# Kernel optimization log

Measured on AMD Instinct MI355X. Metric: run time of the kernel, lower is better.

## Reference

```python
import jax, jax.numpy as jnp
import numpy as np

C = 512        # channels
CTX = 768      # context_dim


def setup_inputs() -> dict:
    key = jax.random.key(0)
    ks = jax.random.split(key, 10)
    B, H, W = 8, 64, 64
    Lc = 512
    s = 0.02
    return {
        "x": jax.random.normal(ks[0], (B, C, H, W), jnp.float32),
        "context": jax.random.normal(ks[1], (B, Lc, CTX), jnp.float32),
        "Wq": jax.random.normal(ks[2], (C, C), jnp.float32) * s,
        "bq": jnp.zeros((C,), jnp.float32),
        "Wk": jax.random.normal(ks[3], (CTX, C), jnp.float32) * s,
        "bk": jnp.zeros((C,), jnp.float32),
        "Wv": jax.random.normal(ks[4], (CTX, C), jnp.float32) * s,
        "bv": jnp.zeros((C,), jnp.float32),
        "Wo": jax.random.normal(ks[5], (C, C), jnp.float32) * s,
        "bo": jnp.zeros((C,), jnp.float32),
    }


def reference(x, context, Wq, bq, Wk, bk, Wv, bv, Wo, bo):
    B, Cdim, H, W = x.shape
    scale = Cdim ** (-0.5)
    # [B, HW, C]
    xr = x.reshape(B, Cdim, H * W).transpose(0, 2, 1)
    q = xr @ Wq + bq                      # [B, HW, C]
    k = context @ Wk + bk                 # [B, Lc, C]
    v = context @ Wv + bv                 # [B, Lc, C]
    sim = jnp.einsum('bqc,bkc->bqk', q, k) * scale
    attn = jax.nn.softmax(sim, axis=-1)
    out = jnp.einsum('bqk,bkc->bqc', attn, v)
    out = out @ Wo + bo                   # [B, HW, C]
    out = out.transpose(0, 2, 1).reshape(B, Cdim, H, W)
    return x + out
```

## Files before the change

### kernel.cpp

```cpp
#include <hip/hip_runtime.h>
#include <hip/hip_bf16.h>

typedef __bf16 bf16_t;
typedef bf16_t bf16x8 __attribute__((ext_vector_type(8)));
typedef bf16_t bf16x4 __attribute__((ext_vector_type(4)));
typedef float  f32x4  __attribute__((ext_vector_type(4)));

constexpr int B_ = 8, C_ = 512, HW_ = 4096, LC_ = 512, CTX_ = 768;


__global__ void k_transpose_w3(const float* __restrict__ Wq, const float* __restrict__ Wk,
                               const float* __restrict__ Wo,
                               bf16_t* __restrict__ Wq_t, bf16_t* __restrict__ Wk_t,
                               bf16_t* __restrict__ Wo_t) {
    __shared__ float t[32][33];
    int zz = blockIdx.z;
    const float* in = (zz == 0) ? Wq : (zz == 1) ? Wk : Wo;
    bf16_t* out     = (zz == 0) ? Wq_t : (zz == 1) ? Wk_t : Wo_t;
    int R = (zz == 1) ? CTX_ : C_;
    int r0 = blockIdx.x * 32, c0 = blockIdx.y * 32;
    if (r0 >= R) return;
    int tx = threadIdx.x, ty = threadIdx.y;
#pragma unroll
    for (int i = 0; i < 4; ++i)
        t[ty + i * 8][tx] = in[(size_t)(r0 + ty + i * 8) * C_ + c0 + tx];
    __syncthreads();
#pragma unroll
    for (int i = 0; i < 4; ++i)
        out[(size_t)(c0 + ty + i * 8) * R + r0 + tx] = (bf16_t)t[tx][ty + i * 8];
}

__global__ void k_bias(const float* __restrict__ bk, const float* __restrict__ bv,
                       const bf16_t* __restrict__ Wo_t, const float* __restrict__ bo,
                       float* __restrict__ bkvo) {
    int blk = blockIdx.x, tid = threadIdx.x;
    if (blk >= 128) {
        int i = (blk - 128) * 256 + tid;
        bkvo[i] = bk[i];
        return;
    }
    int wave = tid >> 6, lane = tid & 63;
    int cc = blk * 4 + wave;
    bf16x8 w = *(const bf16x8*)&Wo_t[(size_t)cc * C_ + lane * 8];
    float s = 0.f;
#pragma unroll
    for (int j = 0; j < 8; ++j) s += bv[lane * 8 + j] * (float)w[j];
#pragma unroll
    for (int o = 32; o > 0; o >>= 1) s += __shfl_xor(s, o);
    if (lane == 0) bkvo[512 + cc] = s + bo[cc];
}

__global__ void k_f32_to_bf16(const float* __restrict__ in, bf16_t* __restrict__ out, int n) {
    int i = (blockIdx.x * 256 + threadIdx.x) * 4;
    if (i >= n) return;
    f32x4 v = *(const f32x4*)(in + i);
    bf16x4 w;
    w[0] = (bf16_t)v.x; w[1] = (bf16_t)v.y; w[2] = (bf16_t)v.z; w[3] = (bf16_t)v.w;
    *(bf16x4*)(out + i) = w;
}

template <int MODE>
__global__ __launch_bounds__(256) void k_gemm(
    const bf16_t* __restrict__ A, int lda, long sA,
    const bf16_t* __restrict__ Bt, int ldb, long sB,
    const float* __restrict__ bias,
    void* __restrict__ out_, long sOut,
    int N, int K, float scale) {
    __shared__ bf16_t lA[128 * 32];
    __shared__ bf16_t lB[128 * 32];
    const int z = blockIdx.z;
    A  += (size_t)z * sA;
    Bt += (size_t)z * sB;
    const int tid  = threadIdx.x;
    const int lane = tid & 63;
    const int wave = tid >> 6;
    const int wm = (wave >> 1) * 64, wn = (wave & 1) * 64;
    const int bm0 = blockIdx.y * 128, bn0 = blockIdx.x * 128;
    const int ar = lane & 15, kc = lane >> 4;

    auto lA3 = (__attribute__((address_space(3))) char*)&lA[0];
    auto lB3 = (__attribute__((address_space(3))) char*)&lB[0];

    f32x4 acc[4][4] = {};

    for (int k0 = 0; k0 < K; k0 += 32) {
        __syncthreads();
#pragma unroll
        for (int s = 0; s < 2; ++s) {
            int wchunk = wave * 2 + s;
            int id = wchunk * 64 + lane;
            int row = id >> 2, c4 = id & 3;
            __builtin_amdgcn_global_load_lds(
                (const __attribute__((address_space(1))) void*)
                    &A[(size_t)(bm0 + row) * lda + k0 + c4 * 8],
                (__attribute__((address_space(3))) void*)(lA3 + wchunk * 1024),
                16, 0, 0);
            __builtin_amdgcn_global_load_lds(
                (const __attribute__((address_space(1))) void*)
                    &Bt[(size_t)(bn0 + row) * ldb + k0 + c4 * 8],
                (__attribute__((address_space(3))) void*)(lB3 + wchunk * 1024),
                16, 0, 0);
        }
        __syncthreads();
        bf16x8 af[4], bfr[4];
#pragma unroll
        for (int f = 0; f < 4; ++f) {
            af[f]  = *(const bf16x8*)&lA[(wm + f * 16 + ar) * 32 + kc * 8];
            bfr[f] = *(const bf16x8*)&lB[(wn + f * 16 + ar) * 32 + kc * 8];
        }
#pragma unroll
        for (int fm = 0; fm < 4; ++fm)
#pragma unroll
            for (int fn = 0; fn < 4; ++fn)
                acc[fm][fn] = __builtin_amdgcn_mfma_f32_16x16x32_bf16(
                    af[fm], bfr[fn], acc[fm][fn], 0, 0, 0);
    }

    const int rj = (lane >> 4) * 4;
    const int cj = lane & 15;

#pragma unroll
    for (int fm = 0; fm < 4; ++fm) {
#pragma unroll
        for (int fn = 0; fn < 4; ++fn) {
            int r0 = bm0 + wm + fm * 16 + rj;
            int cc = bn0 + wn + fn * 16 + cj;
            if constexpr (MODE == 3) {
                bf16_t* out = (bf16_t*)out_;
                bf16x4 v;
#pragma unroll
                for (int j = 0; j < 4; ++j) v[j] = (bf16_t)acc[fm][fn][j];
                *(bf16x4*)&out[(size_t)cc * sOut + r0] = v;
            } else {
                float bb = bias[cc];
                if (cc < 512) {
                    bf16_t* o = (bf16_t*)out_;
#pragma unroll
                    for (int j = 0; j < 4; ++j)
                        o[(size_t)(r0 + j) * 512 + cc] = (bf16_t)(acc[fm][fn][j] + bb);
                } else {
                    bf16_t* o = (bf16_t*)out_ + (size_t)B_ * LC_ * C_;
                    int b = r0 >> 9, l0 = r0 & 511;
                    bf16x4 v;
#pragma unroll
                    for (int j = 0; j < 4; ++j) v[j] = (bf16_t)(acc[fm][fn][j] + bb);
                    *(bf16x4*)&o[((size_t)b * C_ + (cc - 512)) * LC_ + l0] = v;
                }
            }
        }
    }
}

#define SWZ(c16, row) ((((c16)) & 56) | (((c16) ^ (row) ^ ((row) >> 3)) & 7))
__global__ __launch_bounds__(512, 2) void k_flash(
    const bf16_t* __restrict__ Wq_t, const float* __restrict__ bq,
    const bf16_t* __restrict__ Kb, const bf16_t* __restrict__ Vt,
    const float* __restrict__ x, float* __restrict__ out) {
    __shared__ bf16_t lQP[64 * 512];
    __shared__ bf16_t lS[3][16384];
    float (*redA)[64] = (float(*)[64])&lQP[0];
    float (*redB)[64] = (float(*)[64])&lQP[1024];

    const int bid = blockIdx.x;
    const int z = bid & 7;
    const int q0 = (bid >> 3) * 64;
    const int tid = threadIdx.x;
    const int lane = tid & 63;
    const int wave = tid >> 6;
    const int wm2 = wave >> 2;
    const int wn4 = wave & 3;
    const int h = lane >> 4;
    const int r15 = lane & 15;

    const bf16_t* Kz = Kb + (size_t)z * LC_ * C_;
    const bf16_t* Vz = Vt + (size_t)z * C_ * LC_;
    const float*  xz = x + (size_t)z * C_ * HW_;

    auto lS3 = (__attribute__((address_space(3))) char*)&lS[0][0];

    auto STAGE = [&](int b, const bf16_t* __restrict__ src, int t) {
#pragma unroll
        for (int s = 0; s < 4; ++s) {
            int id = s * 512 + tid;
            int row = id >> 2, c4 = id & 3;
            int c4s = c4 ^ ((row >> 1) & 3);
            __builtin_amdgcn_global_load_lds(
                (const __attribute__((address_space(1))) void*)
                    &src[(size_t)row * 512 + t * 32 + c4s * 8],
                (__attribute__((address_space(3))) void*)
                    (lS3 + b * 32768 + s * 8192 + wave * 1024),
                16, 0, 0);
        }
    };

    f32x4 acc[2][8];

    auto PHASE = [&](const bf16_t* __restrict__ src, int off) {
        for (int t = 0; t < 16; ++t) {
            if (t <= 13) STAGE((t + 2 + off) % 3, src, t + 2);
            bf16x8 af[2], bfr[8];
            int c16 = t * 4 + h;
#pragma unroll
            for (int m = 0; m < 2; ++m) {
                int row = wm2 * 32 + m * 16 + r15;
                af[m] = *(const bf16x8*)&lQP[row * 512 + SWZ(c16, row) * 8];
            }
            const bf16_t* lb = &lS[(t + off) % 3][0];
#pragma unroll
            for (int n = 0; n < 8; ++n) {
                int row = wn4 * 128 + n * 16 + r15;
                bfr[n] = *(const bf16x8*)&lb[row * 32 + ((h ^ (row >> 1)) & 3) * 8];
            }
            __builtin_amdgcn_s_setprio(1);
#pragma unroll
            for (int m = 0; m < 2; ++m)
#pragma unroll
                for (int n = 0; n < 8; ++n)
                    acc[m][n] = __builtin_amdgcn_mfma_f32_16x16x32_bf16(
                        af[m], bfr[n], acc[m][n], 0, 0, 0);
            __builtin_amdgcn_s_setprio(0);
            if (t < 15) {
                if (t <= 13) asm volatile("s_waitcnt vmcnt(4)" ::: "memory");
                else         asm volatile("s_waitcnt vmcnt(0)" ::: "memory");
                __builtin_amdgcn_sched_barrier(0);
                __builtin_amdgcn_s_barrier();
                __builtin_amdgcn_sched_barrier(0);
            }
        }
    };

    STAGE(0, Wq_t, 0); STAGE(1, Wq_t, 1);
#pragma unroll
    for (int i = 0; i < 16; ++i) {
        int c = i * 32 + (tid >> 4);
        int q = (tid & 15) * 4;
        f32x4 v = *(const f32x4*)&xz[(size_t)c * HW_ + q0 + q];
        int c16 = c >> 3;
#pragma unroll
        for (int j = 0; j < 4; ++j) {
            int row = q + j;
            lQP[row * 512 + SWZ(c16, row) * 8 + (c & 7)] = (bf16_t)v[j];
        }
    }
    __syncthreads();

#pragma unroll
    for (int m = 0; m < 2; ++m)
#pragma unroll
        for (int n = 0; n < 8; ++n) acc[m][n] = (f32x4)0.f;
    PHASE(Wq_t, 0);

    __syncthreads();
    STAGE(1, Kz, 0); STAGE(2, Kz, 1);
    {
        float bqv[8];
#pragma unroll
        for (int n = 0; n < 8; ++n) bqv[n] = bq[wn4 * 128 + n * 16 + r15];
#pragma unroll
        for (int m = 0; m < 2; ++m)
#pragma unroll
            for (int j = 0; j < 4; ++j) {
                int row = wm2 * 32 + m * 16 + h * 4 + j;
#pragma unroll
                for (int n = 0; n < 8; ++n) {
                    int col = wn4 * 128 + n * 16 + r15;
                    int c16 = col >> 3;
                    lQP[row * 512 + SWZ(c16, row) * 8 + (col & 7)] =
                        (bf16_t)(acc[m][n][j] + bqv[n]);
                }
            }
    }
    __syncthreads();

#pragma unroll
    for (int m = 0; m < 2; ++m)
#pragma unroll
        for (int n = 0; n < 8; ++n) acc[m][n] = (f32x4)0.f;
    PHASE(Kz, 1);

    __syncthreads();
    STAGE(2, Vz, 0); STAGE(0, Vz, 1);
    const float scale = 0.044194173824159216f;
    float M[2][4], inv[2][4];
#pragma unroll
    for (int m = 0; m < 2; ++m)
#pragma unroll
        for (int j = 0; j < 4; ++j) {
            float v = -1e30f;
#pragma unroll
            for (int n = 0; n < 8; ++n) v = fmaxf(v, acc[m][n][j]);
#pragma unroll
            for (int o = 1; o < 16; o <<= 1) v = fmaxf(v, __shfl_xor(v, o));
            if (r15 == 0) redA[wn4][wm2 * 32 + m * 16 + h * 4 + j] = v;
        }
    __syncthreads();
#pragma unroll
    for (int m = 0; m < 2; ++m)
#pragma unroll
        for (int j = 0; j < 4; ++j) {
            int row = wm2 * 32 + m * 16 + h * 4 + j;
            M[m][j] = fmaxf(fmaxf(redA[0][row], redA[1][row]),
                            fmaxf(redA[2][row], redA[3][row]));
        }
#pragma unroll
    for (int m = 0; m < 2; ++m)
#pragma unroll
        for (int j = 0; j < 4; ++j) {
            float s = 0.f;
#pragma unroll
            for (int n = 0; n < 8; ++n) {
                float e = __expf((acc[m][n][j] - M[m][j]) * scale);
                acc[m][n][j] = e;
                s += e;
            }
#pragma unroll
            for (int o = 1; o < 16; o <<= 1) s += __shfl_xor(s, o);
            if (r15 == 0) redB[wn4][wm2 * 32 + m * 16 + h * 4 + j] = s;
        }
    __syncthreads();
#pragma unroll
    for (int m = 0; m < 2; ++m)
#pragma unroll
        for (int j = 0; j < 4; ++j) {
            int row = wm2 * 32 + m * 16 + h * 4 + j;
            inv[m][j] = 1.f / (redB[0][row] + redB[1][row] +
                               redB[2][row] + redB[3][row]);
        }
    __syncthreads();
#pragma unroll
    for (int m = 0; m < 2; ++m)
#pragma unroll
        for (int j = 0; j < 4; ++j) {
            int row = wm2 * 32 + m * 16 + h * 4 + j;
#pragma unroll
            for (int n = 0; n < 8; ++n) {
                int col = wn4 * 128 + n * 16 + r15;
                int c16 = col >> 3;
                lQP[row * 512 + SWZ(c16, row) * 8 + (col & 7)] =
                    (bf16_t)(acc[m][n][j] * inv[m][j]);
            }
        }
    __syncthreads();

#pragma unroll
    for (int m = 0; m < 2; ++m)
#pragma unroll
        for (int n = 0; n < 8; ++n) acc[m][n] = (f32x4)0.f;
    PHASE(Vz, 2);

    float* oz = out + (size_t)z * C_ * HW_;
#pragma unroll
    for (int m = 0; m < 2; ++m)
#pragma unroll
        for (int n = 0; n < 8; ++n) {
            int r0 = q0 + wm2 * 32 + m * 16 + h * 4;
            int cc = wn4 * 128 + n * 16 + r15;
            f32x4 xv = *(const f32x4*)&xz[(size_t)cc * HW_ + r0];
            f32x4 o;
#pragma unroll
            for (int j = 0; j < 4; ++j) o[j] = acc[m][n][j] + xv[j];
            *(f32x4*)&oz[(size_t)cc * HW_ + r0] = o;
        }
}

extern "C" void kernel_launch(void* const* d_in, const int* in_sizes, int n_in,
                              void* d_out, int out_size, void* d_ws, size_t ws_size,
                              hipStream_t stream) {
    (void)in_sizes; (void)n_in; (void)out_size; (void)ws_size;
    const float* x   = (const float*)d_in[0];
    const float* ctx = (const float*)d_in[1];
    const float* Wq  = (const float*)d_in[2];
    const float* bq  = (const float*)d_in[3];
    const float* Wk  = (const float*)d_in[4];
    const float* bk  = (const float*)d_in[5];
    const float* Wv  = (const float*)d_in[6];
    const float* bv  = (const float*)d_in[7];
    const float* Wo  = (const float*)d_in[8];
    const float* bo  = (const float*)d_in[9];
    float* out = (float*)d_out;

    char* ws = (char*)d_ws;
    size_t off = 0;
    auto alloc = [&](size_t bytes) {
        char* p = ws + off;
        off += (bytes + 255) & ~(size_t)255;
        return p;
    };
    bf16_t* Wq_t  = (bf16_t*)alloc((size_t)C_ * C_ * 2);
    bf16_t* Wk_t  = (bf16_t*)alloc((size_t)C_ * CTX_ * 2);
    bf16_t* Wvo_t = (bf16_t*)alloc((size_t)C_ * CTX_ * 2);
    bf16_t* Wv_b  = (bf16_t*)alloc((size_t)CTX_ * C_ * 2);
    bf16_t* Wo_t  = (bf16_t*)alloc((size_t)C_ * C_ * 2);
    float*  bkvo  = (float*)alloc((size_t)1024 * 4);
    bf16_t* ctxb  = (bf16_t*)alloc((size_t)B_ * LC_ * CTX_ * 2);
    bf16_t* Kb    = (bf16_t*)alloc((size_t)B_ * LC_ * C_ * 2);
    bf16_t* Vt    = (bf16_t*)alloc((size_t)B_ * C_ * LC_ * 2);

    k_transpose_w3<<<dim3(CTX_ / 32, C_ / 32, 3), dim3(32, 8), 0, stream>>>(
        Wq, Wk, Wo, Wq_t, Wk_t, Wo_t);
    k_f32_to_bf16<<<(CTX_ * C_ / 4 + 255) / 256, 256, 0, stream>>>(Wv, Wv_b, CTX_ * C_);
    k_bias<<<130, 256, 0, stream>>>(bk, bv, Wo_t, bo, bkvo);
    k_f32_to_bf16<<<(B_ * LC_ * CTX_ / 4 + 255) / 256, 256, 0, stream>>>(
        ctx, ctxb, B_ * LC_ * CTX_);

    k_gemm<3><<<dim3(4, 6, 1), 256, 0, stream>>>(
        Wv_b, C_, 0, Wo_t, C_, 0, nullptr, Wvo_t, CTX_, C_, C_, 1.f);
    k_gemm<4><<<dim3(8, 32, 1), 256, 0, stream>>>(
        ctxb, CTX_, 0, Wk_t, CTX_, 0, bkvo, Kb, 0, 1024, CTX_, 1.f);
    k_flash<<<512, 512, 0, stream>>>(Wq_t, bq, Kb, Vt, x, out);
}
```

Before: 188.6 us.

## Load B operands directly from global into registers, drop LDS staging

Replaces the triple-buffered LDS staging of the Wq/K/V tiles, done with global_load_lds plus per-step barriers, with direct per-wave global loads into registers, double-buffered across k-steps. This frees 96KB of LDS and removes the block barriers inside each phase. In exchange, each wave now fetches its own B fragments from global/L2 with no sharing across waves in the block, so global traffic and register pressure go up. The launch-bounds occupancy hint of 2 is dropped.

Measured after the change: 280.1 us. 1.49x slower.

```diff
diff --git a/kernel.cpp b/kernel.cpp
--- a/kernel.cpp
+++ b/kernel.cpp
@@ -152,12 +152,11 @@
 }
 
 #define SWZ(c16, row) ((((c16)) & 56) | (((c16) ^ (row) ^ ((row) >> 3)) & 7))
-__global__ __launch_bounds__(512, 2) void k_flash(
+__global__ __launch_bounds__(512) void k_flash(
     const bf16_t* __restrict__ Wq_t, const float* __restrict__ bq,
     const bf16_t* __restrict__ Kb, const bf16_t* __restrict__ Vt,
     const float* __restrict__ x, float* __restrict__ out) {
     __shared__ bf16_t lQP[64 * 512];
-    __shared__ bf16_t lS[3][16384];
     float (*redA)[64] = (float(*)[64])&lQP[0];
     float (*redB)[64] = (float(*)[64])&lQP[1024];
 
@@ -176,60 +175,64 @@
     const bf16_t* Vz = Vt + (size_t)z * C_ * LC_;
     const float*  xz = x + (size_t)z * C_ * HW_;
 
-    auto lS3 = (__attribute__((address_space(3))) char*)&lS[0][0];
-
-    auto STAGE = [&](int b, const bf16_t* __restrict__ src, int t) {
-#pragma unroll
-        for (int s = 0; s < 4; ++s) {
-            int id = s * 512 + tid;
-            int row = id >> 2, c4 = id & 3;
-            int c4s = c4 ^ ((row >> 1) & 3);
-            __builtin_amdgcn_global_load_lds(
-                (const __attribute__((address_space(1))) void*)
-                    &src[(size_t)row * 512 + t * 32 + c4s * 8],
-                (__attribute__((address_space(3))) void*)
-                    (lS3 + b * 32768 + s * 8192 + wave * 1024),
-                16, 0, 0);
+    f32x4 acc[2][8];
+
+    auto PHASE = [&](const bf16_t* __restrict__ src) {
+        const bf16_t* bp[8];
+#pragma unroll
+        for (int n = 0; n < 8; ++n)
+            bp[n] = src + (size_t)(wn4 * 128 + n * 16 + r15) * 512 + h * 8;
+        bf16x8 b0[8], b1[8];
+#pragma unroll
+        for (int n = 0; n < 8; ++n) b0[n] = *(const bf16x8*)(bp[n]);
+#pragma unroll
+        for (int tt = 0; tt < 8; ++tt) {
+            const int t = 2 * tt;
+#pragma unroll
+            for (int n = 0; n < 8; ++n)
+                b1[n] = *(const bf16x8*)(bp[n] + (t + 1) * 32);
+            {
+                bf16x8 af[2];
+                int c16 = t * 4 + h;
+#pragma unroll
+                for (int m = 0; m < 2; ++m) {
+                    int row = wm2 * 32 + m * 16 + r15;
+                    af[m] = *(const bf16x8*)&lQP[row * 512 + SWZ(c16, row) * 8];
+                }
+                __builtin_amdgcn_s_setprio(1);
+#pragma unroll
+                for (int m = 0; m < 2; ++m)
+#pragma unroll
+                    for (int n = 0; n < 8; ++n)
+                        acc[m][n] = __builtin_amdgcn_mfma_f32_16x16x32_bf16(
+                            af[m], b0[n], acc[m][n], 0, 0, 0);
+                __builtin_amdgcn_s_setprio(0);
+            }
+            if (t + 2 < 16) {
+#pragma unroll
+                for (int n = 0; n < 8; ++n)
+                    b0[n] = *(const bf16x8*)(bp[n] + (t + 2) * 32);
+            }
+            {
+                bf16x8 af[2];
+                int c16 = (t + 1) * 4 + h;
+#pragma unroll
+                for (int m = 0; m < 2; ++m) {
+                    int row = wm2 * 32 + m * 16 + r15;
+                    af[m] = *(const bf16x8*)&lQP[row * 512 + SWZ(c16, row) * 8];
+                }
+                __builtin_amdgcn_s_setprio(1);
+#pragma unroll
+                for (int m = 0; m < 2; ++m)
+#pragma unroll
+                    for (int n = 0; n < 8; ++n)
+                        acc[m][n] = __builtin_amdgcn_mfma_f32_16x16x32_bf16(
+                            af[m], b1[n], acc[m][n], 0, 0, 0);
+                __builtin_amdgcn_s_setprio(0);
+            }
         }
     };
 
-    f32x4 acc[2][8];
-
-    auto PHASE = [&](const bf16_t* __restrict__ src, int off) {
-        for (int t = 0; t < 16; ++t) {
-            if (t <= 13) STAGE((t + 2 + off) % 3, src, t + 2);
-            bf16x8 af[2], bfr[8];
-            int c16 = t * 4 + h;
-#pragma unroll
-            for (int m = 0; m < 2; ++m) {
-                int row = wm2 * 32 + m * 16 + r15;
-                af[m] = *(const bf16x8*)&lQP[row * 512 + SWZ(c16, row) * 8];
-            }
-            const bf16_t* lb = &lS[(t + off) % 3][0];
-#pragma unroll
-            for (int n = 0; n < 8; ++n) {
-                int row = wn4 * 128 + n * 16 + r15;
-                bfr[n] = *(const bf16x8*)&lb[row * 32 + ((h ^ (row >> 1)) & 3) * 8];
-            }
-            __builtin_amdgcn_s_setprio(1);
-#pragma unroll
-            for (int m = 0; m < 2; ++m)
-#pragma unroll
-                for (int n = 0; n < 8; ++n)
-                    acc[m][n] = __builtin_amdgcn_mfma_f32_16x16x32_bf16(
-                        af[m], bfr[n], acc[m][n], 0, 0, 0);
-            __builtin_amdgcn_s_setprio(0);
-            if (t < 15) {
-                if (t <= 13) asm volatile("s_waitcnt vmcnt(4)" ::: "memory");
-                else         asm volatile("s_waitcnt vmcnt(0)" ::: "memory");
-                __builtin_amdgcn_sched_barrier(0);
-                __builtin_amdgcn_s_barrier();
-                __builtin_amdgcn_sched_barrier(0);
-            }
-        }
-    };
-
-    STAGE(0, Wq_t, 0); STAGE(1, Wq_t, 1);
 #pragma unroll
     for (int i = 0; i < 16; ++i) {
         int c = i * 32 + (tid >> 4);
@@ -248,10 +251,9 @@
     for (int m = 0; m < 2; ++m)
 #pragma unroll
         for (int n = 0; n < 8; ++n) acc[m][n] = (f32x4)0.f;
-    PHASE(Wq_t, 0);
-
-    __syncthreads();
-    STAGE(1, Kz, 0); STAGE(2, Kz, 1);
+    PHASE(Wq_t);
+
+    __syncthreads();
     {
         float bqv[8];
 #pragma unroll
@@ -276,10 +278,9 @@
     for (int m = 0; m < 2; ++m)
 #pragma unroll
         for (int n = 0; n < 8; ++n) acc[m][n] = (f32x4)0.f;
-    PHASE(Kz, 1);
-
-    __syncthreads();
-    STAGE(2, Vz, 0); STAGE(0, Vz, 1);
+    PHASE(Kz);
+
+    __syncthreads();
     const float scale = 0.044194173824159216f;
     float M[2][4], inv[2][4];
 #pragma unroll
@@ -346,7 +347,7 @@
     for (int m = 0; m < 2; ++m)
 #pragma unroll
         for (int n = 0; n < 8; ++n) acc[m][n] = (f32x4)0.f;
-    PHASE(Vz, 2);
+    PHASE(Vz);
 
     float* oz = out + (size_t)z * C_ * HW_;
 #pragma unroll
```
